# Optimization experiments

Hardware: AMD Instinct MI355X
Metric: run time of the kernel (lower is better)

Reference implementation:

```python
import math
import jax, jax.numpy as jnp
import numpy as np

B, S, D, H, V = 8, 1024, 512, 8, 32000
HD = D // H


def _position_embedding(seq_len, d_model):
    pos = jnp.arange(seq_len, dtype=jnp.float32)[:, None]                 # [S,1]
    div = jnp.exp(jnp.arange(0, d_model, 2, dtype=jnp.float32) * (-math.log(10000.0) / d_model))  # [D/2]
    ang = pos * div                                                        # [S,D/2]
    # interleave sin (even cols) / cos (odd cols)
    return jnp.stack([jnp.sin(ang), jnp.cos(ang)], axis=-1).reshape(seq_len, d_model)


def _min_max_normalize(w):
    lo = jnp.min(w, axis=-1, keepdims=True)
    hi = jnp.max(w, axis=-1, keepdims=True)
    return (w - lo) / (hi - lo)


def _converable_mask(h, Wc, bc):
    bs, seq = h.shape[0], h.shape[1]
    half = seq // 2
    shift = math.ceil(seq / 2)
    width = jnp.einsum('bsd,od->bso', h, Wc)[..., 0] + bc[0]               # [B,S]
    width = _min_max_normalize(width)[..., None]                           # [B,S,1]
    origin = jnp.concatenate([jnp.linspace(1.0, 0.0, half),
                              jnp.linspace(0.0, 1.0, seq - half)])         # [S]
    origin_mask = 1.0 - jax.nn.sigmoid((origin[None, None, :] - width) * 100.0)  # [B,S,S]
    idx = (jnp.arange(seq - 1, -1, -1)[:, None] + jnp.arange(seq)[None, :]) % seq  # [S,S]
    idx = jnp.roll(idx, shift, axis=0)
    # torch.roll of a [1,S] row along dim 0 is a no-op
    cmp = idx >= jnp.arange(seq)[None, :]                                  # [S,S] bool
    move = jnp.concatenate([cmp[:shift], ~cmp[shift:]], axis=0)            # [S,S]
    gathered = jnp.take_along_axis(origin_mask, idx[None, :, :], axis=2)   # [B,S,S]
    return gathered * move.astype(origin_mask.dtype)


def setup_inputs():
    key = jax.random.key(0)
    ks = jax.random.split(key, 9)
    s_emb = 1.0
    s_hd = 1.0 / math.sqrt(HD)
    s_d = 1.0 / math.sqrt(D)
    return {
        'x':   jax.random.randint(ks[0], (B, S), 0, V),
        'emb': jax.random.normal(ks[1], (V, D), dtype=jnp.float32) * s_emb,
        'Wq':  jax.random.normal(ks[2], (HD, HD), dtype=jnp.float32) * s_hd,
        'Wk':  jax.random.normal(ks[3], (HD, HD), dtype=jnp.float32) * s_hd,
        'Wv':  jax.random.normal(ks[4], (HD, HD), dtype=jnp.float32) * s_hd,
        'Wo':  jax.random.normal(ks[5], (D, D), dtype=jnp.float32) * s_d,
        'bo':  jnp.zeros((D,), dtype=jnp.float32),
        'Wc':  jax.random.normal(ks[6], (1, D), dtype=jnp.float32) * s_d,
        'bc':  jnp.zeros((1,), dtype=jnp.float32),
    }


def reference(x, emb, Wq, Wk, Wv, Wo, bo, Wc, bc):
    h = emb[x] + _position_embedding(S, D)[None]                           # [B,S,D]
    mask = _converable_mask(h, Wc, bc)                                     # [B,S,S]
    hh = h.reshape(B, S, H, HD)
    q = jnp.einsum('bshd,od->bsho', hh, Wq)
    k = jnp.einsum('bshd,od->bsho', hh, Wk)
    v = jnp.einsum('bshd,od->bsho', hh, Wv)
    energy = jnp.einsum('bqhd,bkhd->bhqk', q, k)                           # [B,H,S,S]
    # mask [B,S,S] broadcasts as [1,B,S,S]; valid because B == H (as in original)
    energy = energy * mask
    attn = jax.nn.softmax(energy / math.sqrt(D), axis=3)
    out = jnp.einsum('bhqk,bkhd->bqhd', attn, v).reshape(B, S, D)
    out = out @ Wo.T + bo
    return (out, mask)
```

## Files before the change

kernel.cpp:

```cpp
#include <hip/hip_runtime.h>
#include <hip/hip_bf16.h>
#include <math.h>

#define Bn 8
#define Sn 1024
#define Dn 512
#define Hn 8
#define HDn 64

typedef __bf16 bf16x8 __attribute__((ext_vector_type(8)));
typedef __bf16 bf16x4 __attribute__((ext_vector_type(4)));
typedef float  f32x4  __attribute__((ext_vector_type(4)));

__global__ void k_embed(const int* __restrict__ x, const float* __restrict__ emb,
                        float* __restrict__ h) {
    const int total = Bn * Sn * Dn;
    for (int i = blockIdx.x * blockDim.x + threadIdx.x; i < total; i += gridDim.x * blockDim.x) {
        int d = i & (Dn - 1);
        int bs = i >> 9;
        int s = bs & (Sn - 1);
        int tok = x[bs];
        float f = __expf((float)(d & ~1) * (-9.210340371976184f / 512.0f));
        float ang = (float)s * f;
        float pe = (d & 1) ? __cosf(ang) : __sinf(ang);
        h[i] = emb[(size_t)tok * Dn + d] + pe;
    }
}

__global__ void k_width(const float* __restrict__ h, const float* __restrict__ Wc,
                        const float* __restrict__ bc, float* __restrict__ width) {
    int row = blockIdx.x * 4 + (threadIdx.x >> 6);
    int lane = threadIdx.x & 63;
    const float* hr = h + (size_t)row * Dn;
    float acc = 0.f;
    for (int i = lane; i < Dn; i += 64) acc += hr[i] * Wc[i];
    for (int off = 32; off > 0; off >>= 1) acc += __shfl_down(acc, off);
    if (lane == 0) width[row] = acc + bc[0];
}

__global__ void k_minmax(const float* __restrict__ width, float* __restrict__ lo,
                         float* __restrict__ hi) {
    int b = blockIdx.x;
    __shared__ float smin[256], smax[256];
    float mn = 1e30f, mx = -1e30f;
    for (int s = threadIdx.x; s < Sn; s += 256) {
        float v = width[b * Sn + s];
        mn = fminf(mn, v);
        mx = fmaxf(mx, v);
    }
    smin[threadIdx.x] = mn; smax[threadIdx.x] = mx;
    __syncthreads();
    for (int off = 128; off; off >>= 1) {
        if (threadIdx.x < off) {
            smin[threadIdx.x] = fminf(smin[threadIdx.x], smin[threadIdx.x + off]);
            smax[threadIdx.x] = fmaxf(smax[threadIdx.x], smax[threadIdx.x + off]);
        }
        __syncthreads();
    }
    if (threadIdx.x == 0) { lo[b] = smin[0]; hi[b] = smax[0]; }
}

__global__ void k_mask(const float* __restrict__ width, const float* __restrict__ lo,
                       const float* __restrict__ hi, float* __restrict__ mask_out,
                       __bf16* __restrict__ maskb) {
    const float SCALE = 0.04419417382415922f;
    int bs = blockIdx.x;
    int b = bs >> 10;
    int s = bs & (Sn - 1);
    float wn = (width[bs] - lo[b]) / (hi[b] - lo[b]);
    for (int t = threadIdx.x; t < Sn; t += 256) {
        int it = (t - s + 1535) & (Sn - 1);
        float origin = (it < 512) ? (1.0f - (float)it * (1.0f / 511.0f))
                                  : ((float)(it - 512) * (1.0f / 511.0f));
        float z = (origin - wn) * 100.0f;
        float om;
        if (z >= 0.0f) { float e = __expf(-z); om = e / (1.0f + e); }
        else           { float e = __expf(z);  om = 1.0f / (1.0f + e); }
        bool cmpv = (it >= t);
        bool mv = (s < 512) ? cmpv : !cmpv;
        float val = mv ? om : 0.0f;
        mask_out[(size_t)bs * Sn + t] = val;
        maskb[(size_t)bs * Sn + t] = (__bf16)(val * SCALE);
    }
}

__global__ __launch_bounds__(256) void k_qkv(
        const float* __restrict__ h, const float* __restrict__ Wq,
        const float* __restrict__ Wk, const float* __restrict__ Wv,
        __bf16* __restrict__ q, __bf16* __restrict__ k, __bf16* __restrict__ vt) {
    __shared__ __align__(16) __bf16 Xs[64][72];
    __shared__ __align__(16) __bf16 WqS[64][72];
    __shared__ __align__(16) __bf16 WkS[64][72];
    __shared__ __align__(16) __bf16 WvS[64][72];
    int t = threadIdx.x;
    int m0 = blockIdx.x * 64;
    int w = t >> 6, lane = t & 63, quad = lane >> 4, li = lane & 15;

    #pragma unroll
    for (int it = 0; it < 4; ++it) {
        int e = (it * 256 + t) * 4; int r = e >> 6, c = e & 63;
        float4 xv = *(const float4*)&h[(size_t)(m0 + r) * 64 + c];
        *(bf16x4*)&Xs[r][c]  = (bf16x4){(__bf16)xv.x, (__bf16)xv.y, (__bf16)xv.z, (__bf16)xv.w};
        float4 qv = *(const float4*)&Wq[e];
        *(bf16x4*)&WqS[r][c] = (bf16x4){(__bf16)qv.x, (__bf16)qv.y, (__bf16)qv.z, (__bf16)qv.w};
        float4 kv = *(const float4*)&Wk[e];
        *(bf16x4*)&WkS[r][c] = (bf16x4){(__bf16)kv.x, (__bf16)kv.y, (__bf16)kv.z, (__bf16)kv.w};
        float4 vv = *(const float4*)&Wv[e];
        *(bf16x4*)&WvS[r][c] = (bf16x4){(__bf16)vv.x, (__bf16)vv.y, (__bf16)vv.z, (__bf16)vv.w};
    }
    __syncthreads();

    bf16x8 A0 = *(const bf16x8*)&Xs[w * 16 + li][quad * 8];
    bf16x8 A1 = *(const bf16x8*)&Xs[w * 16 + li][32 + quad * 8];
    f32x4 aq[4], ak[4], av[4];
    #pragma unroll
    for (int n = 0; n < 4; ++n) {
        aq[n] = (f32x4){0.f,0.f,0.f,0.f}; ak[n] = aq[n]; av[n] = aq[n];
        bf16x8 Bq0 = *(const bf16x8*)&WqS[n * 16 + li][quad * 8];
        bf16x8 Bq1 = *(const bf16x8*)&WqS[n * 16 + li][32 + quad * 8];
        aq[n] = __builtin_amdgcn_mfma_f32_16x16x32_bf16(A0, Bq0, aq[n], 0, 0, 0);
        aq[n] = __builtin_amdgcn_mfma_f32_16x16x32_bf16(A1, Bq1, aq[n], 0, 0, 0);
        bf16x8 Bk0 = *(const bf16x8*)&WkS[n * 16 + li][quad * 8];
        bf16x8 Bk1 = *(const bf16x8*)&WkS[n * 16 + li][32 + quad * 8];
        ak[n] = __builtin_amdgcn_mfma_f32_16x16x32_bf16(A0, Bk0, ak[n], 0, 0, 0);
        ak[n] = __builtin_amdgcn_mfma_f32_16x16x32_bf16(A1, Bk1, ak[n], 0, 0, 0);
        bf16x8 Bv0 = *(const bf16x8*)&WvS[n * 16 + li][quad * 8];
        bf16x8 Bv1 = *(const bf16x8*)&WvS[n * 16 + li][32 + quad * 8];
        av[n] = __builtin_amdgcn_mfma_f32_16x16x32_bf16(A0, Bv0, av[n], 0, 0, 0);
        av[n] = __builtin_amdgcn_mfma_f32_16x16x32_bf16(A1, Bv1, av[n], 0, 0, 0);
    }

    #pragma unroll
    for (int n = 0; n < 4; ++n)
        #pragma unroll
        for (int r = 0; r < 4; ++r) {
            int Rg = m0 + w * 16 + quad * 4 + r;
            int bsI = Rg >> 3, head = Rg & 7;
            int b = bsI >> 10, s = bsI & (Sn - 1);
            size_t oidx = (((size_t)(b * Hn + head)) * Sn + s) * HDn + n * 16 + li;
            q[oidx] = (__bf16)aq[n][r];
            k[oidx] = (__bf16)ak[n][r];
        }

    __bf16 (*Vs)[72] = WqS;
    __syncthreads();
    #pragma unroll
    for (int n = 0; n < 4; ++n)
        #pragma unroll
        for (int r = 0; r < 4; ++r)
            Vs[w * 16 + quad * 4 + r][n * 16 + li] = (__bf16)av[n][r];
    __syncthreads();
    int bs0 = m0 >> 3;
    int b = bs0 >> 10, s0l = bs0 & (Sn - 1);
    #pragma unroll
    for (int i = 0; i < 2; ++i) {
        int p = t + 256 * i;
        int head = p >> 6, o = p & 63;
        __bf16 tmp[8];
        #pragma unroll
        for (int j = 0; j < 8; ++j) tmp[j] = Vs[j * 8 + head][o];
        *(bf16x8*)&vt[(((size_t)(b * Hn + head)) * HDn + o) * Sn + s0l] = *(bf16x8*)tmp;
    }
}

__global__ __launch_bounds__(256) void k_attn(
        const __bf16* __restrict__ q, const __bf16* __restrict__ k,
        const __bf16* __restrict__ vt, const __bf16* __restrict__ maskb,
        __bf16* __restrict__ ao) {
    __shared__ __align__(16) __bf16 Ks[64][72];
    __shared__ __align__(16) __bf16 Vt[64][72];
    __shared__ __align__(16) __bf16 Ps[64][76];
    __shared__ __align__(16) __bf16 Ms[64][76];
    int blk = blockIdx.x;
    int hh = blk & 7;
    int qt = (blk >> 3) & 15;
    int b  = blk >> 7;
    int bh = b * Hn + hh;
    int q0 = qt * 64;
    int t = threadIdx.x;
    int w = t >> 6, lane = t & 63, quad = lane >> 4, li = lane & 15;

    const __bf16* qbase  = q  + ((size_t)bh * Sn + q0) * HDn;
    const __bf16* kbase  = k  + (size_t)bh * Sn * HDn;
    const __bf16* vtbase = vt + (size_t)bh * HDn * Sn;
    const __bf16* mbase  = maskb + ((size_t)hh * Sn + q0) * Sn;

    bf16x8 A0 = *(const bf16x8*)&qbase[(w * 16 + li) * HDn + quad * 8];
    bf16x8 A1 = *(const bf16x8*)&qbase[(w * 16 + li) * HDn + 32 + quad * 8];

    f32x4 O[4];
    #pragma unroll
    for (int n = 0; n < 4; ++n) O[n] = (f32x4){0.f, 0.f, 0.f, 0.f};
    float rs[4] = {0.f, 0.f, 0.f, 0.f};

    for (int k0 = 0; k0 < Sn; k0 += 64) {
        if (k0) __syncthreads();
        #pragma unroll
        for (int it = 0; it < 2; ++it) {
            int e = (it * 256 + t) * 8; int r = e >> 6, c = e & 63;
            *(bf16x8*)&Ks[r][c] = *(const bf16x8*)&kbase[(size_t)k0 * HDn + e];
            *(bf16x8*)&Vt[r][c] = *(const bf16x8*)&vtbase[(size_t)r * Sn + k0 + c];
            *(bf16x8*)&Ms[r][c] = *(const bf16x8*)&mbase[(size_t)r * Sn + k0 + c];
        }
        __syncthreads();

        f32x4 Sf[4];
        #pragma unroll
        for (int n = 0; n < 4; ++n) {
            f32x4 acc = (f32x4){0.f, 0.f, 0.f, 0.f};
            bf16x8 B0 = *(const bf16x8*)&Ks[n * 16 + li][quad * 8];
            acc = __builtin_amdgcn_mfma_f32_16x16x32_bf16(A0, B0, acc, 0, 0, 0);
            bf16x8 B1 = *(const bf16x8*)&Ks[n * 16 + li][32 + quad * 8];
            acc = __builtin_amdgcn_mfma_f32_16x16x32_bf16(A1, B1, acc, 0, 0, 0);
            Sf[n] = acc;
        }

        #pragma unroll
        for (int n = 0; n < 4; ++n)
            #pragma unroll
            for (int r = 0; r < 4; ++r) {
                float sv = Sf[n][r] * (float)Ms[w * 16 + quad * 4 + r][n * 16 + li];
                float p = __expf(sv);
                rs[r] += p;
                Ps[w * 16 + quad * 4 + r][n * 16 + li] = (__bf16)p;
            }

        #pragma unroll
        for (int kc = 0; kc < 2; ++kc) {
            bf16x8 Ap = *(const bf16x8*)&Ps[w * 16 + li][kc * 32 + quad * 8];
            #pragma unroll
            for (int n = 0; n < 4; ++n) {
                bf16x8 Bv = *(const bf16x8*)&Vt[n * 16 + li][kc * 32 + quad * 8];
                O[n] = __builtin_amdgcn_mfma_f32_16x16x32_bf16(Ap, Bv, O[n], 0, 0, 0);
            }
        }
    }

    #pragma unroll
    for (int off = 1; off < 16; off <<= 1)
        #pragma unroll
        for (int r = 0; r < 4; ++r) rs[r] += __shfl_xor(rs[r], off);
    float inv[4];
    #pragma unroll
    for (int r = 0; r < 4; ++r) inv[r] = __fdividef(1.0f, rs[r]);
    #pragma unroll
    for (int n = 0; n < 4; ++n)
        #pragma unroll
        for (int r = 0; r < 4; ++r)
            ao[((size_t)b * Sn + q0 + w * 16 + quad * 4 + r) * Dn + hh * HDn + n * 16 + li]
                = (__bf16)(O[n][r] * inv[r]);
}

__global__ __launch_bounds__(256) void k_proj(
        const __bf16* __restrict__ ao, const float* __restrict__ Wo,
        const float* __restrict__ bo, float* __restrict__ out) {
    __shared__ __align__(16) __bf16 As[64][72];
    __shared__ __align__(16) __bf16 Bs[64][72];
    int bm = blockIdx.x >> 3;
    int bn = blockIdx.x & 7;
    int m0 = bm * 64, n0 = bn * 64;
    int t = threadIdx.x;
    int w = t >> 6, lane = t & 63, quad = lane >> 4, li = lane & 15;

    f32x4 O[4];
    #pragma unroll
    for (int n = 0; n < 4; ++n) O[n] = (f32x4){0.f, 0.f, 0.f, 0.f};

    for (int k0 = 0; k0 < Dn; k0 += 64) {
        if (k0) __syncthreads();
        #pragma unroll
        for (int it = 0; it < 2; ++it) {
            int e = (it * 256 + t) * 8; int r = e >> 6, c = e & 63;
            *(bf16x8*)&As[r][c] = *(const bf16x8*)&ao[(size_t)(m0 + r) * Dn + k0 + c];
        }
        #pragma unroll
        for (int it = 0; it < 4; ++it) {
            int e = (it * 256 + t) * 4; int r = e >> 6, c = e & 63;
            float4 wv = *(const float4*)&Wo[(size_t)(n0 + r) * Dn + k0 + c];
            *(bf16x4*)&Bs[r][c] = (bf16x4){(__bf16)wv.x, (__bf16)wv.y, (__bf16)wv.z, (__bf16)wv.w};
        }
        __syncthreads();

        bf16x8 A0 = *(const bf16x8*)&As[w * 16 + li][quad * 8];
        bf16x8 A1 = *(const bf16x8*)&As[w * 16 + li][32 + quad * 8];
        #pragma unroll
        for (int n = 0; n < 4; ++n) {
            bf16x8 B0 = *(const bf16x8*)&Bs[n * 16 + li][quad * 8];
            O[n] = __builtin_amdgcn_mfma_f32_16x16x32_bf16(A0, B0, O[n], 0, 0, 0);
            bf16x8 B1 = *(const bf16x8*)&Bs[n * 16 + li][32 + quad * 8];
            O[n] = __builtin_amdgcn_mfma_f32_16x16x32_bf16(A1, B1, O[n], 0, 0, 0);
        }
    }

    #pragma unroll
    for (int n = 0; n < 4; ++n) {
        float bias = bo[n0 + n * 16 + li];
        #pragma unroll
        for (int r = 0; r < 4; ++r)
            out[(size_t)(m0 + w * 16 + quad * 4 + r) * Dn + n0 + n * 16 + li] = O[n][r] + bias;
    }
}

extern "C" void kernel_launch(void* const* d_in, const int* in_sizes, int n_in,
                              void* d_out, int out_size, void* d_ws, size_t ws_size,
                              hipStream_t stream) {
    const int*   x   = (const int*)d_in[0];
    const float* emb = (const float*)d_in[1];
    const float* Wq  = (const float*)d_in[2];
    const float* Wk  = (const float*)d_in[3];
    const float* Wv  = (const float*)d_in[4];
    const float* Wo  = (const float*)d_in[5];
    const float* bo  = (const float*)d_in[6];
    const float* Wc  = (const float*)d_in[7];
    const float* bc  = (const float*)d_in[8];

    float* ws    = (float*)d_ws;
    float* h     = ws;
    float* width = h + (size_t)Bn * Sn * Dn;
    float* lo    = width + Bn * Sn;
    float* hi    = lo + Bn;
    __bf16* qb   = (__bf16*)(hi + Bn);
    __bf16* kb   = qb + (size_t)Bn * Sn * Dn;
    __bf16* vtb  = kb + (size_t)Bn * Sn * Dn;
    __bf16* maskb = vtb + (size_t)Bn * Sn * Dn;
    __bf16* ao   = (__bf16*)h;

    float* out      = (float*)d_out;
    float* mask_out = out + (size_t)Bn * Sn * Dn;

    k_embed<<<4096, 256, 0, stream>>>(x, emb, h);
    k_width<<<(Bn * Sn) / 4, 256, 0, stream>>>(h, Wc, bc, width);
    k_minmax<<<Bn, 256, 0, stream>>>(width, lo, hi);
    k_mask<<<Bn * Sn, 256, 0, stream>>>(width, lo, hi, mask_out, maskb);
    k_qkv<<<(Bn * Sn * Hn) / 64, 256, 0, stream>>>(h, Wq, Wk, Wv, qb, kb, vtb);
    k_attn<<<Bn * Hn * (Sn / 64), 256, 0, stream>>>(qb, kb, vtb, maskb, ao);
    k_proj<<<(Bn * Sn / 64) * (Dn / 64), 256, 0, stream>>>(ao, Wo, bo, out);
}
```

Before: 223.7 us.

## Fuse embedding, width and min-max into QKV kernel; prefetch K/V in attention

Embedding lookup, positional encoding, the width dot product and the per-batch min/max reduction are folded into the QKV projection kernel. Min/max now uses order-preserving integer atomics, so the fp32 h tensor is never written to or read back from global memory and three launches go away. The attention kernel register-prefetches the next K/V tile while the current one is processed, and reads mask values straight from global memory instead of staging them in LDS. This adds a memset launch, atomic contention on 16 words, and uncoalesced-ish per-row mask loads.

Result: faster. 207.7 us (-7.1%).

```diff
diff --git a/kernel.cpp b/kernel.cpp
--- a/kernel.cpp
+++ b/kernel.cpp
@@ -12,95 +12,64 @@
 typedef __bf16 bf16x4 __attribute__((ext_vector_type(4)));
 typedef float  f32x4  __attribute__((ext_vector_type(4)));
 
-__global__ void k_embed(const int* __restrict__ x, const float* __restrict__ emb,
-                        float* __restrict__ h) {
-    const int total = Bn * Sn * Dn;
-    for (int i = blockIdx.x * blockDim.x + threadIdx.x; i < total; i += gridDim.x * blockDim.x) {
-        int d = i & (Dn - 1);
-        int bs = i >> 9;
-        int s = bs & (Sn - 1);
-        int tok = x[bs];
-        float f = __expf((float)(d & ~1) * (-9.210340371976184f / 512.0f));
-        float ang = (float)s * f;
-        float pe = (d & 1) ? __cosf(ang) : __sinf(ang);
-        h[i] = emb[(size_t)tok * Dn + d] + pe;
-    }
-}
-
-__global__ void k_width(const float* __restrict__ h, const float* __restrict__ Wc,
-                        const float* __restrict__ bc, float* __restrict__ width) {
-    int row = blockIdx.x * 4 + (threadIdx.x >> 6);
-    int lane = threadIdx.x & 63;
-    const float* hr = h + (size_t)row * Dn;
-    float acc = 0.f;
-    for (int i = lane; i < Dn; i += 64) acc += hr[i] * Wc[i];
-    for (int off = 32; off > 0; off >>= 1) acc += __shfl_down(acc, off);
-    if (lane == 0) width[row] = acc + bc[0];
-}
-
-__global__ void k_minmax(const float* __restrict__ width, float* __restrict__ lo,
-                         float* __restrict__ hi) {
-    int b = blockIdx.x;
-    __shared__ float smin[256], smax[256];
-    float mn = 1e30f, mx = -1e30f;
-    for (int s = threadIdx.x; s < Sn; s += 256) {
-        float v = width[b * Sn + s];
-        mn = fminf(mn, v);
-        mx = fmaxf(mx, v);
-    }
-    smin[threadIdx.x] = mn; smax[threadIdx.x] = mx;
-    __syncthreads();
-    for (int off = 128; off; off >>= 1) {
-        if (threadIdx.x < off) {
-            smin[threadIdx.x] = fminf(smin[threadIdx.x], smin[threadIdx.x + off]);
-            smax[threadIdx.x] = fmaxf(smax[threadIdx.x], smax[threadIdx.x + off]);
-        }
-        __syncthreads();
-    }
-    if (threadIdx.x == 0) { lo[b] = smin[0]; hi[b] = smax[0]; }
-}
-
-__global__ void k_mask(const float* __restrict__ width, const float* __restrict__ lo,
-                       const float* __restrict__ hi, float* __restrict__ mask_out,
-                       __bf16* __restrict__ maskb) {
-    const float SCALE = 0.04419417382415922f;
-    int bs = blockIdx.x;
-    int b = bs >> 10;
-    int s = bs & (Sn - 1);
-    float wn = (width[bs] - lo[b]) / (hi[b] - lo[b]);
-    for (int t = threadIdx.x; t < Sn; t += 256) {
-        int it = (t - s + 1535) & (Sn - 1);
-        float origin = (it < 512) ? (1.0f - (float)it * (1.0f / 511.0f))
-                                  : ((float)(it - 512) * (1.0f / 511.0f));
-        float z = (origin - wn) * 100.0f;
-        float om;
-        if (z >= 0.0f) { float e = __expf(-z); om = e / (1.0f + e); }
-        else           { float e = __expf(z);  om = 1.0f / (1.0f + e); }
-        bool cmpv = (it >= t);
-        bool mv = (s < 512) ? cmpv : !cmpv;
-        float val = mv ? om : 0.0f;
-        mask_out[(size_t)bs * Sn + t] = val;
-        maskb[(size_t)bs * Sn + t] = (__bf16)(val * SCALE);
-    }
-}
-
-__global__ __launch_bounds__(256) void k_qkv(
-        const float* __restrict__ h, const float* __restrict__ Wq,
-        const float* __restrict__ Wk, const float* __restrict__ Wv,
+__device__ __forceinline__ unsigned enc_f(float v) {
+    unsigned u = __float_as_uint(v);
+    return (u & 0x80000000u) ? ~u : (u | 0x80000000u);
+}
+__device__ __forceinline__ float dec_f(unsigned k) {
+    unsigned u = (k & 0x80000000u) ? (k ^ 0x80000000u) : ~k;
+    return __uint_as_float(u);
+}
+
+__global__ __launch_bounds__(256) void k_fused(
+        const int* __restrict__ x, const float* __restrict__ emb,
+        const float* __restrict__ Wc, const float* __restrict__ bc,
+        const float* __restrict__ Wq, const float* __restrict__ Wk,
+        const float* __restrict__ Wv,
+        float* __restrict__ width, unsigned* __restrict__ lohi,
         __bf16* __restrict__ q, __bf16* __restrict__ k, __bf16* __restrict__ vt) {
     __shared__ __align__(16) __bf16 Xs[64][72];
     __shared__ __align__(16) __bf16 WqS[64][72];
     __shared__ __align__(16) __bf16 WkS[64][72];
     __shared__ __align__(16) __bf16 WvS[64][72];
+    __shared__ float wtok[8];
     int t = threadIdx.x;
+    int bs0 = blockIdx.x * 8;
     int m0 = blockIdx.x * 64;
     int w = t >> 6, lane = t & 63, quad = lane >> 4, li = lane & 15;
 
+    {
+        int token = t >> 5, l32 = t & 31;
+        int bs = bs0 + token;
+        int s = bs & (Sn - 1);
+        int tok = x[bs];
+        float wpart = 0.f;
+        int row = token * 8 + ((l32 * 16) >> 6);
+        #pragma unroll
+        for (int j = 0; j < 4; ++j) {
+            int d0 = l32 * 16 + j * 4;
+            float4 ev = *(const float4*)&emb[(size_t)tok * Dn + d0];
+            float4 wc = *(const float4*)&Wc[d0];
+            float hv[4];
+            #pragma unroll
+            for (int i = 0; i < 4; ++i) {
+                int d = d0 + i;
+                float f = __expf((float)(d & ~1) * (-9.210340371976184f / 512.0f));
+                float ang = (float)s * f;
+                float pe = (d & 1) ? __cosf(ang) : __sinf(ang);
+                hv[i] = (&ev.x)[i] + pe;
+                wpart += hv[i] * (&wc.x)[i];
+            }
+            *(bf16x4*)&Xs[row][d0 & 63] =
+                (bf16x4){(__bf16)hv[0], (__bf16)hv[1], (__bf16)hv[2], (__bf16)hv[3]};
+        }
+        #pragma unroll
+        for (int off = 1; off < 32; off <<= 1) wpart += __shfl_xor(wpart, off);
+        if (l32 == 0) { float wv = wpart + bc[0]; width[bs] = wv; wtok[token] = wv; }
+    }
     #pragma unroll
     for (int it = 0; it < 4; ++it) {
         int e = (it * 256 + t) * 4; int r = e >> 6, c = e & 63;
-        float4 xv = *(const float4*)&h[(size_t)(m0 + r) * 64 + c];
-        *(bf16x4*)&Xs[r][c]  = (bf16x4){(__bf16)xv.x, (__bf16)xv.y, (__bf16)xv.z, (__bf16)xv.w};
         float4 qv = *(const float4*)&Wq[e];
         *(bf16x4*)&WqS[r][c] = (bf16x4){(__bf16)qv.x, (__bf16)qv.y, (__bf16)qv.z, (__bf16)qv.w};
         float4 kv = *(const float4*)&Wk[e];
@@ -109,6 +78,15 @@
         *(bf16x4*)&WvS[r][c] = (bf16x4){(__bf16)vv.x, (__bf16)vv.y, (__bf16)vv.z, (__bf16)vv.w};
     }
     __syncthreads();
+
+    if (t == 0) {
+        float mn = wtok[0], mx = wtok[0];
+        #pragma unroll
+        for (int i = 1; i < 8; ++i) { mn = fminf(mn, wtok[i]); mx = fmaxf(mx, wtok[i]); }
+        int b = bs0 >> 10;
+        atomicMin(&lohi[b], enc_f(mn));
+        atomicMin(&lohi[8 + b], ~enc_f(mx));
+    }
 
     bf16x8 A0 = *(const bf16x8*)&Xs[w * 16 + li][quad * 8];
     bf16x8 A1 = *(const bf16x8*)&Xs[w * 16 + li][32 + quad * 8];
@@ -150,8 +128,8 @@
         for (int r = 0; r < 4; ++r)
             Vs[w * 16 + quad * 4 + r][n * 16 + li] = (__bf16)av[n][r];
     __syncthreads();
-    int bs0 = m0 >> 3;
-    int b = bs0 >> 10, s0l = bs0 & (Sn - 1);
+    int bs0i = m0 >> 3;
+    int b = bs0i >> 10, s0l = bs0i & (Sn - 1);
     #pragma unroll
     for (int i = 0; i < 2; ++i) {
         int p = t + 256 * i;
@@ -160,6 +138,31 @@
         #pragma unroll
         for (int j = 0; j < 8; ++j) tmp[j] = Vs[j * 8 + head][o];
         *(bf16x8*)&vt[(((size_t)(b * Hn + head)) * HDn + o) * Sn + s0l] = *(bf16x8*)tmp;
+    }
+}
+
+__global__ void k_mask(const float* __restrict__ width, const unsigned* __restrict__ lohi,
+                       float* __restrict__ mask_out, __bf16* __restrict__ maskb) {
+    const float SCALE = 0.04419417382415922f;
+    int bs = blockIdx.x;
+    int b = bs >> 10;
+    int s = bs & (Sn - 1);
+    float lo = dec_f(lohi[b]);
+    float hi = dec_f(~lohi[8 + b]);
+    float wn = (width[bs] - lo) / (hi - lo);
+    for (int t = threadIdx.x; t < Sn; t += 256) {
+        int it = (t - s + 1535) & (Sn - 1);
+        float origin = (it < 512) ? (1.0f - (float)it * (1.0f / 511.0f))
+                                  : ((float)(it - 512) * (1.0f / 511.0f));
+        float z = (origin - wn) * 100.0f;
+        float om;
+        if (z >= 0.0f) { float e = __expf(-z); om = e / (1.0f + e); }
+        else           { float e = __expf(z);  om = 1.0f / (1.0f + e); }
+        bool cmpv = (it >= t);
+        bool mv = (s < 512) ? cmpv : !cmpv;
+        float val = mv ? om : 0.0f;
+        mask_out[(size_t)bs * Sn + t] = val;
+        maskb[(size_t)bs * Sn + t] = (__bf16)(val * SCALE);
     }
 }
 
@@ -170,7 +173,6 @@
     __shared__ __align__(16) __bf16 Ks[64][72];
     __shared__ __align__(16) __bf16 Vt[64][72];
     __shared__ __align__(16) __bf16 Ps[64][76];
-    __shared__ __align__(16) __bf16 Ms[64][76];
     int blk = blockIdx.x;
     int hh = blk & 7;
     int qt = (blk >> 3) & 15;
@@ -183,11 +185,22 @@
     const __bf16* qbase  = q  + ((size_t)bh * Sn + q0) * HDn;
     const __bf16* kbase  = k  + (size_t)bh * Sn * HDn;
     const __bf16* vtbase = vt + (size_t)bh * HDn * Sn;
-    const __bf16* mbase  = maskb + ((size_t)hh * Sn + q0) * Sn;
+    const __bf16* mrow[4];
+    #pragma unroll
+    for (int r = 0; r < 4; ++r)
+        mrow[r] = maskb + ((size_t)hh * Sn + q0 + w * 16 + quad * 4 + r) * Sn;
 
     bf16x8 A0 = *(const bf16x8*)&qbase[(w * 16 + li) * HDn + quad * 8];
     bf16x8 A1 = *(const bf16x8*)&qbase[(w * 16 + li) * HDn + 32 + quad * 8];
 
+    bf16x8 pk[2], pv[2];
+    #pragma unroll
+    for (int it = 0; it < 2; ++it) {
+        int e = (it * 256 + t) * 8; int r = e >> 6, c = e & 63;
+        pk[it] = *(const bf16x8*)&kbase[e];
+        pv[it] = *(const bf16x8*)&vtbase[(size_t)r * Sn + c];
+    }
+
     f32x4 O[4];
     #pragma unroll
     for (int n = 0; n < 4; ++n) O[n] = (f32x4){0.f, 0.f, 0.f, 0.f};
@@ -198,11 +211,25 @@
         #pragma unroll
         for (int it = 0; it < 2; ++it) {
             int e = (it * 256 + t) * 8; int r = e >> 6, c = e & 63;
-            *(bf16x8*)&Ks[r][c] = *(const bf16x8*)&kbase[(size_t)k0 * HDn + e];
-            *(bf16x8*)&Vt[r][c] = *(const bf16x8*)&vtbase[(size_t)r * Sn + k0 + c];
-            *(bf16x8*)&Ms[r][c] = *(const bf16x8*)&mbase[(size_t)r * Sn + k0 + c];
+            *(bf16x8*)&Ks[r][c] = pk[it];
+            *(bf16x8*)&Vt[r][c] = pv[it];
         }
         __syncthreads();
+        if (k0 + 64 < Sn) {
+            #pragma unroll
+            for (int it = 0; it < 2; ++it) {
+                int e = (it * 256 + t) * 8; int r = e >> 6, c = e & 63;
+                pk[it] = *(const bf16x8*)&kbase[(size_t)(k0 + 64) * HDn + e];
+                pv[it] = *(const bf16x8*)&vtbase[(size_t)r * Sn + (k0 + 64) + c];
+            }
+        }
+
+        float msk[4][4];
+        #pragma unroll
+        for (int n = 0; n < 4; ++n)
+            #pragma unroll
+            for (int r = 0; r < 4; ++r)
+                msk[n][r] = (float)mrow[r][k0 + n * 16 + li];
 
         f32x4 Sf[4];
         #pragma unroll
@@ -219,8 +246,7 @@
         for (int n = 0; n < 4; ++n)
             #pragma unroll
             for (int r = 0; r < 4; ++r) {
-                float sv = Sf[n][r] * (float)Ms[w * 16 + quad * 4 + r][n * 16 + li];
-                float p = __expf(sv);
+                float p = __expf(Sf[n][r] * msk[n][r]);
                 rs[r] += p;
                 Ps[w * 16 + quad * 4 + r][n * 16 + li] = (__bf16)p;
             }
@@ -314,25 +340,22 @@
     const float* Wc  = (const float*)d_in[7];
     const float* bc  = (const float*)d_in[8];
 
-    float* ws    = (float*)d_ws;
-    float* h     = ws;
-    float* width = h + (size_t)Bn * Sn * Dn;
-    float* lo    = width + Bn * Sn;
-    float* hi    = lo + Bn;
-    __bf16* qb   = (__bf16*)(hi + Bn);
+    float* ws      = (float*)d_ws;
+    float* width   = ws;
+    unsigned* lohi = (unsigned*)(width + Bn * Sn);
+    __bf16* qb   = (__bf16*)(ws + Bn * Sn + 16);
     __bf16* kb   = qb + (size_t)Bn * Sn * Dn;
     __bf16* vtb  = kb + (size_t)Bn * Sn * Dn;
     __bf16* maskb = vtb + (size_t)Bn * Sn * Dn;
-    __bf16* ao   = (__bf16*)h;
+    __bf16* ao   = maskb + (size_t)Bn * Sn * Sn;
 
     float* out      = (float*)d_out;
     float* mask_out = out + (size_t)Bn * Sn * Dn;
 
-    k_embed<<<4096, 256, 0, stream>>>(x, emb, h);
-    k_width<<<(Bn * Sn) / 4, 256, 0, stream>>>(h, Wc, bc, width);
-    k_minmax<<<Bn, 256, 0, stream>>>(width, lo, hi);
-    k_mask<<<Bn * Sn, 256, 0, stream>>>(width, lo, hi, mask_out, maskb);
-    k_qkv<<<(Bn * Sn * Hn) / 64, 256, 0, stream>>>(h, Wq, Wk, Wv, qb, kb, vtb);
+    hipMemsetAsync(lohi, 0xFF, 16 * sizeof(unsigned), stream);
+    k_fused<<<(Bn * Sn) / 8, 256, 0, stream>>>(x, emb, Wc, bc, Wq, Wk, Wv,
+                                               width, lohi, qb, kb, vtb);
+    k_mask<<<Bn * Sn, 256, 0, stream>>>(width, lohi, mask_out, maskb);
     k_attn<<<Bn * Hn * (Sn / 64), 256, 0, stream>>>(qb, kb, vtb, maskb, ao);
     k_proj<<<(Bn * Sn / 64) * (Dn / 64), 256, 0, stream>>>(ao, Wo, bo, out);
 }
```
